# Kernel optimization log

Measured on AMD Instinct MI355X. Metric: run time of the kernel, lower is better.

The kernel has to match this reference:

```python
import jax, jax.numpy as jnp
import numpy as np

K_SIZE = 2
STRIDE = 2
PAD = 0
EPS = 1e-8


def setup_inputs() -> dict:
    key = jax.random.key(0)
    # (batch, quat_groups, 4, H, W)
    x = jax.random.normal(key, (8, 64, 4, 128, 128), dtype=jnp.float32)
    return {"x": x}


def _unfold(x, k, s, p):
    """Replicates F.unfold patch extraction on (B,G,4,H,W).
    Returns (B, G, 4, k*k, L) with unfold's (kernel-row, kernel-col) ordering,
    plus H_out, W_out."""
    B, G, Q, H, W = x.shape
    xp = jnp.pad(x, ((0, 0), (0, 0), (0, 0), (p, p), (p, p)))
    Ho = (H + 2 * p - k) // s + 1
    Wo = (W + 2 * p - k) // s + 1
    patches = []
    for i in range(k):          # fixed small kernel loop (k*k = 4)
        for j in range(k):
            patches.append(xp[:, :, :, i:i + s * Ho:s, j:j + s * Wo:s])
    u = jnp.stack(patches, axis=3)            # (B,G,4,k*k,Ho,Wo)
    return u.reshape(B, G, Q, k * k, Ho * Wo), Ho, Wo


def reference(x):
    B, G, Q, H, W = x.shape
    u, Ho, Wo = _unfold(x, K_SIZE, STRIDE, PAD)     # (B,G,4,K,L)
    # per-window quaternion magnitude
    mag = jnp.sqrt(jnp.sum(u * u, axis=2))          # (B,G,K,L)
    # NOTE: faithful to source — normalization is over the L (output-position)
    # axis (dim=3), entropy summed over kernel-area axis (dim=2)
    p = mag / (jnp.sum(mag, axis=3, keepdims=True) + EPS)
    ent = -jnp.sum(p * jnp.log(p + EPS), axis=2)    # (B,G,L)
    idx = jnp.argmax(ent, axis=1)                   # (B,L), first max like torch
    # gather max-entropy quaternion group per output position
    sel = jnp.take_along_axis(u, idx[:, None, None, None, :], axis=1)[:, 0]  # (B,4,K,L)
    pooled = jnp.transpose(sel, (0, 3, 1, 2))       # (B,L,4,K) matches torch adv-index layout
    return pooled.reshape(B, -1, Ho, Wo)            # (B, 4*K, Ho, Wo), faithful quirky view
```

## Files before the change

kernel.cpp:

```cpp
#include <hip/hip_runtime.h>
#include <math.h>

#define NB 8
#define NG 64
#define NQ 4
#define NH 128
#define NW 128
#define NL 4096
#define EPSF 1e-8f

#define WINNER_CT (NB * NL)
#define S_CT (NB * NG * 4)
#define MAG_OFF ((size_t)(WINNER_CT + S_CT) * 8)

__global__ __launch_bounds__(256) void mag_kernel(const float4* __restrict__ x4,
                                                  float2* __restrict__ mag2,
                                                  double* __restrict__ S) {
    int t = blockIdx.x * 256 + threadIdx.x;
    int wp = t & 31;
    int ho = (t >> 5) & 63;
    int g  = (t >> 11) & 63;
    int b  = t >> 17;

    long base4 = (long)((b * NG + g) * NQ) * (NH * NW / 4);
    float sqA[4] = {0.f, 0.f, 0.f, 0.f};
    float sqB[4] = {0.f, 0.f, 0.f, 0.f};
#pragma unroll
    for (int q = 0; q < NQ; q++) {
#pragma unroll
        for (int i = 0; i < 2; i++) {
            float4 v = x4[base4 + (long)q * (NH * NW / 4) + (2 * ho + i) * (NW / 4) + wp];
            sqA[i * 2]     = __fadd_rn(sqA[i * 2],     __fmul_rn(v.x, v.x));
            sqA[i * 2 + 1] = __fadd_rn(sqA[i * 2 + 1], __fmul_rn(v.y, v.y));
            sqB[i * 2]     = __fadd_rn(sqB[i * 2],     __fmul_rn(v.z, v.z));
            sqB[i * 2 + 1] = __fadd_rn(sqB[i * 2 + 1], __fmul_rn(v.w, v.w));
        }
    }

    int lane = threadIdx.x & 63;
    int sidx = (b * NG + g) * 4;
    long m2base = (long)sidx * (NL / 2) + ho * 32 + wp;
#pragma unroll
    for (int k = 0; k < 4; k++) {
        float mA = __fsqrt_rn(sqA[k]);
        float mB = __fsqrt_rn(sqB[k]);
        mag2[m2base + (long)k * (NL / 2)] = make_float2(mA, mB);
        double d = (double)mA + (double)mB;
#pragma unroll
        for (int off = 32; off; off >>= 1) d += __shfl_xor(d, off, 64);
        if (lane == k * 16) atomicAdd(&S[sidx + k], d);
    }
}

__global__ __launch_bounds__(256) void ent_kernel(const float* __restrict__ mag,
                                                  const double* __restrict__ S,
                                                  unsigned long long* __restrict__ winner) {
    int t = blockIdx.x * 256 + threadIdx.x;
    int l = t & 4095;
    int g = (t >> 12) & 63;
    int b = t >> 18;
    int sidx = (b * NG + g) * 4;

    __shared__ float rcp4[4];
    if (threadIdx.x < 4) {
        float denom = __fadd_rn((float)S[sidx + threadIdx.x], EPSF);
        rcp4[threadIdx.x] = (float)(1.0 / (double)denom);
    }
    __syncthreads();

    long mbase = (long)sidx * NL + l;
    float e = 0.f;
#pragma unroll
    for (int k = 0; k < 4; k++) {
        float p = __fmul_rn(mag[mbase + (long)k * NL], rcp4[k]);
        float lg = logf(__fadd_rn(p, EPSF));
        e = __fadd_rn(e, __fmul_rn(p, lg));
    }
    float f = -e;
    unsigned int bits = __float_as_uint(f);
    unsigned int key = (bits & 0x80000000u) ? ~bits : (bits | 0x80000000u);
    unsigned long long pk = ((unsigned long long)key << 32) | (unsigned long long)(63 - g);
    atomicMax(&winner[b * NL + l], pk);
}

__global__ __launch_bounds__(256) void gather_kernel(const float2* __restrict__ x2,
                                                     const unsigned long long* __restrict__ winner,
                                                     float4* __restrict__ out4) {
    int t = blockIdx.x * 256 + threadIdx.x;
    int q = t & 3;
    int l = (t >> 2) & 4095;
    int b = t >> 14;
    unsigned long long w = winner[b * NL + l];
    int g = 63 - (int)(w & 63ull);
    int ho = l >> 6, wo = l & 63;
    long base2 = (long)((b * NG + g) * NQ + q) * (NH * NW / 2);
    float2 t0 = x2[base2 + (2 * ho) * (NW / 2) + wo];
    float2 t1 = x2[base2 + (2 * ho + 1) * (NW / 2) + wo];
    out4[t] = make_float4(t0.x, t0.y, t1.x, t1.y);
}

extern "C" void kernel_launch(void* const* d_in, const int* in_sizes, int n_in,
                              void* d_out, int out_size, void* d_ws, size_t ws_size,
                              hipStream_t stream) {
    const float* x = (const float*)d_in[0];
    float* out = (float*)d_out;

    unsigned long long* winner = (unsigned long long*)d_ws;
    double* S = (double*)((char*)d_ws + (size_t)WINNER_CT * 8);
    float* mag = (float*)((char*)d_ws + MAG_OFF);

    hipMemsetAsync(d_ws, 0, MAG_OFF, stream);

    mag_kernel<<<(NB * NG * 64 * 32) / 256, 256, 0, stream>>>(
        (const float4*)x, (float2*)mag, S);
    ent_kernel<<<(NB * NG * NL) / 256, 256, 0, stream>>>(mag, S, winner);
    gather_kernel<<<(NB * NL * NQ) / 256, 256, 0, stream>>>(
        (const float2*)x, winner, (float4*)out);
}
```

Measured before the change: 213.0 us.

## Fuse magnitude and entropy kernels with per-block reduction of window sums

Result: no change. 210.5 us (-1.2%).

```diff
diff --git a/kernel.cpp b/kernel.cpp
--- a/kernel.cpp
+++ b/kernel.cpp
@@ -10,77 +10,91 @@
 #define EPSF 1e-8f
 
 #define WINNER_CT (NB * NL)
-#define S_CT (NB * NG * 4)
-#define MAG_OFF ((size_t)(WINNER_CT + S_CT) * 8)
 
-__global__ __launch_bounds__(256) void mag_kernel(const float4* __restrict__ x4,
-                                                  float2* __restrict__ mag2,
-                                                  double* __restrict__ S) {
-    int t = blockIdx.x * 256 + threadIdx.x;
-    int wp = t & 31;
-    int ho = (t >> 5) & 63;
-    int g  = (t >> 11) & 63;
-    int b  = t >> 17;
+__global__ __launch_bounds__(1024) void fused_kernel(const float4* __restrict__ x4,
+                                                     unsigned long long* __restrict__ winner) {
+    int bg = blockIdx.x;
+    int b = bg >> 6;
+    int g = bg & 63;
+    int tid = threadIdx.x;
 
-    long base4 = (long)((b * NG + g) * NQ) * (NH * NW / 4);
-    float sqA[4] = {0.f, 0.f, 0.f, 0.f};
-    float sqB[4] = {0.f, 0.f, 0.f, 0.f};
+    long base4 = (long)(bg * NQ) * (NH * NW / 4);
+
+    float mg[2][2][4];
+    double dsum[4] = {0.0, 0.0, 0.0, 0.0};
 #pragma unroll
-    for (int q = 0; q < NQ; q++) {
+    for (int pp = 0; pp < 2; pp++) {
+        int pos = tid + pp * 1024;
+        int ho = pos >> 5, wp = pos & 31;
+        float sqA[4] = {0.f, 0.f, 0.f, 0.f};
+        float sqB[4] = {0.f, 0.f, 0.f, 0.f};
 #pragma unroll
-        for (int i = 0; i < 2; i++) {
-            float4 v = x4[base4 + (long)q * (NH * NW / 4) + (2 * ho + i) * (NW / 4) + wp];
-            sqA[i * 2]     = __fadd_rn(sqA[i * 2],     __fmul_rn(v.x, v.x));
-            sqA[i * 2 + 1] = __fadd_rn(sqA[i * 2 + 1], __fmul_rn(v.y, v.y));
-            sqB[i * 2]     = __fadd_rn(sqB[i * 2],     __fmul_rn(v.z, v.z));
-            sqB[i * 2 + 1] = __fadd_rn(sqB[i * 2 + 1], __fmul_rn(v.w, v.w));
+        for (int q = 0; q < NQ; q++) {
+#pragma unroll
+            for (int i = 0; i < 2; i++) {
+                float4 v = x4[base4 + (long)q * (NH * NW / 4) + (2 * ho + i) * (NW / 4) + wp];
+                sqA[i * 2]     = __fadd_rn(sqA[i * 2],     __fmul_rn(v.x, v.x));
+                sqA[i * 2 + 1] = __fadd_rn(sqA[i * 2 + 1], __fmul_rn(v.y, v.y));
+                sqB[i * 2]     = __fadd_rn(sqB[i * 2],     __fmul_rn(v.z, v.z));
+                sqB[i * 2 + 1] = __fadd_rn(sqB[i * 2 + 1], __fmul_rn(v.w, v.w));
+            }
+        }
+#pragma unroll
+        for (int k = 0; k < 4; k++) {
+            float mA = __fsqrt_rn(sqA[k]);
+            float mB = __fsqrt_rn(sqB[k]);
+            mg[pp][0][k] = mA;
+            mg[pp][1][k] = mB;
+            dsum[k] += (double)mA + (double)mB;
         }
     }
 
-    int lane = threadIdx.x & 63;
-    int sidx = (b * NG + g) * 4;
-    long m2base = (long)sidx * (NL / 2) + ho * 32 + wp;
 #pragma unroll
     for (int k = 0; k < 4; k++) {
-        float mA = __fsqrt_rn(sqA[k]);
-        float mB = __fsqrt_rn(sqB[k]);
-        mag2[m2base + (long)k * (NL / 2)] = make_float2(mA, mB);
-        double d = (double)mA + (double)mB;
 #pragma unroll
-        for (int off = 32; off; off >>= 1) d += __shfl_xor(d, off, 64);
-        if (lane == k * 16) atomicAdd(&S[sidx + k], d);
+        for (int off = 32; off; off >>= 1) dsum[k] += __shfl_xor(dsum[k], off, 64);
     }
-}
-
-__global__ __launch_bounds__(256) void ent_kernel(const float* __restrict__ mag,
-                                                  const double* __restrict__ S,
-                                                  unsigned long long* __restrict__ winner) {
-    int t = blockIdx.x * 256 + threadIdx.x;
-    int l = t & 4095;
-    int g = (t >> 12) & 63;
-    int b = t >> 18;
-    int sidx = (b * NG + g) * 4;
-
-    __shared__ float rcp4[4];
-    if (threadIdx.x < 4) {
-        float denom = __fadd_rn((float)S[sidx + threadIdx.x], EPSF);
-        rcp4[threadIdx.x] = (float)(1.0 / (double)denom);
+    __shared__ double lds[16][4];
+    __shared__ float rcp4s[4];
+    int wave = tid >> 6, lane = tid & 63;
+    if (lane == 0) {
+#pragma unroll
+        for (int k = 0; k < 4; k++) lds[wave][k] = dsum[k];
     }
     __syncthreads();
+    if (tid < 4) {
+        double s = 0.0;
+        for (int w = 0; w < 16; w++) s += lds[w][tid];
+        float denom = __fadd_rn((float)s, EPSF);
+        rcp4s[tid] = (float)(1.0 / (double)denom);
+    }
+    __syncthreads();
+    float r0 = rcp4s[0], r1 = rcp4s[1], r2 = rcp4s[2], r3 = rcp4s[3];
 
-    long mbase = (long)sidx * NL + l;
-    float e = 0.f;
+    unsigned long long gk = (unsigned long long)(63 - g);
+    unsigned long long* wrow = winner + b * NL;
 #pragma unroll
-    for (int k = 0; k < 4; k++) {
-        float p = __fmul_rn(mag[mbase + (long)k * NL], rcp4[k]);
-        float lg = logf(__fadd_rn(p, EPSF));
-        e = __fadd_rn(e, __fmul_rn(p, lg));
+    for (int pp = 0; pp < 2; pp++) {
+        int pos = tid + pp * 1024;
+        int ho = pos >> 5, wp = pos & 31;
+#pragma unroll
+        for (int w = 0; w < 2; w++) {
+            float p0 = __fmul_rn(mg[pp][w][0], r0);
+            float p1 = __fmul_rn(mg[pp][w][1], r1);
+            float p2 = __fmul_rn(mg[pp][w][2], r2);
+            float p3 = __fmul_rn(mg[pp][w][3], r3);
+            float e = 0.f;
+            e = __fadd_rn(e, __fmul_rn(p0, logf(__fadd_rn(p0, EPSF))));
+            e = __fadd_rn(e, __fmul_rn(p1, logf(__fadd_rn(p1, EPSF))));
+            e = __fadd_rn(e, __fmul_rn(p2, logf(__fadd_rn(p2, EPSF))));
+            e = __fadd_rn(e, __fmul_rn(p3, logf(__fadd_rn(p3, EPSF))));
+            float f = -e;
+            unsigned int bits = __float_as_uint(f);
+            unsigned int key = (bits & 0x80000000u) ? ~bits : (bits | 0x80000000u);
+            int l = ho * 64 + 2 * wp + w;
+            atomicMax(&wrow[l], ((unsigned long long)key << 32) | gk);
+        }
     }
-    float f = -e;
-    unsigned int bits = __float_as_uint(f);
-    unsigned int key = (bits & 0x80000000u) ? ~bits : (bits | 0x80000000u);
-    unsigned long long pk = ((unsigned long long)key << 32) | (unsigned long long)(63 - g);
-    atomicMax(&winner[b * NL + l], pk);
 }
 
 __global__ __launch_bounds__(256) void gather_kernel(const float2* __restrict__ x2,
@@ -104,16 +118,11 @@
                               hipStream_t stream) {
     const float* x = (const float*)d_in[0];
     float* out = (float*)d_out;
+    unsigned long long* winner = (unsigned long long*)d_ws;
 
-    unsigned long long* winner = (unsigned long long*)d_ws;
-    double* S = (double*)((char*)d_ws + (size_t)WINNER_CT * 8);
-    float* mag = (float*)((char*)d_ws + MAG_OFF);
+    hipMemsetAsync(winner, 0, (size_t)WINNER_CT * 8, stream);
 
-    hipMemsetAsync(d_ws, 0, MAG_OFF, stream);
-
-    mag_kernel<<<(NB * NG * 64 * 32) / 256, 256, 0, stream>>>(
-        (const float4*)x, (float2*)mag, S);
-    ent_kernel<<<(NB * NG * NL) / 256, 256, 0, stream>>>(mag, S, winner);
+    fused_kernel<<<NB * NG, 1024, 0, stream>>>((const float4*)x, winner);
     gather_kernel<<<(NB * NL * NQ) / 256, 256, 0, stream>>>(
         (const float2*)x, winner, (float4*)out);
 }
```
